# Kernel tuning notes

Hardware: AMD Instinct MI355X
Metric: run time of the kernel (lower is better)

The kernel has to match this reference:

```python
import jax, jax.numpy as jnp
import numpy as np

B, T, I, H, L = 64, 2048, 128, 128, 2  # batch, seq_len, input, hidden, layers


def setup_inputs() -> dict:
    key = jax.random.key(0)
    ks = jax.random.split(key, 6)
    w = lambda k, shape: jax.random.normal(k, shape, dtype=jnp.float32) * 0.05
    return {
        "x": jax.random.normal(ks[0], (B, T, I), dtype=jnp.float32),
        "Wx0": w(ks[1], (4 * H, I)),
        "Wh0": w(ks[2], (4 * H, H)),
        "b0": jnp.zeros((4 * H,), jnp.float32),
        "Wx1": w(ks[3], (4 * H, H)),
        "Wh1": w(ks[4], (4 * H, H)),
        "b1": jnp.zeros((4 * H,), jnp.float32),
    }


def _cell(x_t, h, c, Wx, Wh, b):
    # fused-gate GEMM; gate order (i, f, g, o) matches the torch cell exactly
    gates = x_t @ Wx.T + h @ Wh.T + b  # [B, 4H]
    i, f, g, o = jnp.split(gates, 4, axis=-1)
    i = jax.nn.sigmoid(i)
    f = jax.nn.sigmoid(f)
    g = jnp.tanh(g)
    o = jax.nn.sigmoid(o)
    c_new = f * c + i * g
    h_new = o * jnp.tanh(c_new)
    return h_new, c_new


def reference(x, Wx0, Wh0, b0, Wx1, Wh1, b1):
    params = [(Wx0, Wh0, b0), (Wx1, Wh1, b1)]
    bsz = x.shape[0]
    hidden = Wh0.shape[1]
    h0 = jnp.zeros((L, bsz, hidden), x.dtype)
    c0 = jnp.zeros((L, bsz, hidden), x.dtype)

    def step(carry, x_t):
        h, c = carry
        hs, cs = [], []
        inp = x_t
        for l, (Wx, Wh, b) in enumerate(params):  # fixed, tiny layer loop
            hl, cl = _cell(inp, h[l], c[l], Wx, Wh, b)
            inp = hl
            hs.append(hl)
            cs.append(cl)
        return (jnp.stack(hs), jnp.stack(cs)), inp

    (hT, cT), ys = jax.lax.scan(step, (h0, c0), jnp.swapaxes(x, 0, 1))
    output = jnp.swapaxes(ys, 0, 1)  # [B, T, H], top-layer hidden states
    return output, hT, cT
```

## Files before the change

kernel.cpp:

```cpp
#include <hip/hip_runtime.h>
#include <hip/hip_fp16.h>

#define BB 64
#define TT 2048
#define II 128
#define HH 128
#define NG 512
#define CH 128
#define NCH (TT / CH)
#define LEAD 4
#define DYN_LDS 81984

typedef _Float16 h2_t __attribute__((ext_vector_type(2)));

#if defined(__has_builtin)
#if __has_builtin(__builtin_amdgcn_fdot2)
#define HAVE_FDOT2 1
#endif
#endif

__device__ __forceinline__ float fdot2f(h2_t a, h2_t b, float c) {
#ifdef HAVE_FDOT2
  return __builtin_amdgcn_fdot2(a, b, c, false);
#else
  return c + (float)a[0] * (float)b[0] + (float)a[1] * (float)b[1];
#endif
}

__device__ __forceinline__ float fast_sigmoid(float x) {
  float t = __builtin_amdgcn_exp2f(-1.4426950408889634f * x);
  return __builtin_amdgcn_rcpf(1.0f + t);
}
__device__ __forceinline__ float act_gate(float x, bool tanh_sel) {
  float xx = tanh_sel ? 2.0f * x : x;
  float s = fast_sigmoid(xx);
  return tanh_sel ? 2.0f * s - 1.0f : s;
}
__device__ __forceinline__ float fast_tanh(float x) {
  return 2.0f * fast_sigmoid(2.0f * x) - 1.0f;
}

__device__ __forceinline__ float dpp_xor1(float x) {
  return __int_as_float(__builtin_amdgcn_update_dpp(0, __float_as_int(x), 0xB1, 0xF, 0xF, true));
}
__device__ __forceinline__ float dpp_xor2(float x) {
  return __int_as_float(__builtin_amdgcn_update_dpp(0, __float_as_int(x), 0x4E, 0xF, 0xF, true));
}

__device__ __forceinline__ void bar_lds() {
  __builtin_amdgcn_fence(__ATOMIC_RELEASE, "workgroup", "local");
  __builtin_amdgcn_s_barrier();
  __builtin_amdgcn_fence(__ATOMIC_ACQUIRE, "workgroup", "local");
}

union LD4 {
  float4 f4;
  h2_t h[4];
};
union LDB {
  uint4 u4;
  h2_t h[4];
};

__device__ __forceinline__ unsigned aload(unsigned* p) { return atomicAdd(p, 0u); }

__global__ void w_transpose2(const float* __restrict__ W0, float* __restrict__ T0,
                             const float* __restrict__ W1, float* __restrict__ T1) {
  int bid = blockIdx.x;
  const float* W = (bid < 256) ? W0 : W1;
  float* T = (bid < 256) ? T0 : T1;
  int idx = (bid & 255) * 256 + threadIdx.x;
  int n = idx >> 7;
  int k = idx & 127;
  T[k * NG + n] = W[idx];
}

__global__ __launch_bounds__(256) void xg_gemm_pro(const float* __restrict__ X,
                                                   const float* __restrict__ WT,
                                                   const float* __restrict__ bias,
                                                   __half* __restrict__ Xg) {
  __shared__ float As[64][132];
  __shared__ float Bs[128][64];
  const int bx = blockIdx.x;
  const size_t m0 = (size_t)(bx >> 3) * TT + (bx & 7) * 64;
  const int n0 = blockIdx.y * 64;
  const int tid = threadIdx.x;

  {
    const float4* xv = (const float4*)(X + m0 * II);
#pragma unroll
    for (int r = 0; r < 8; ++r) {
      int f = tid + 256 * r;
      int m = f >> 5;
      int c4 = f & 31;
      float4 v = xv[m * 32 + c4];
      *(float4*)&As[m][c4 * 4] = v;
    }
  }
  {
#pragma unroll
    for (int r = 0; r < 8; ++r) {
      int f = tid + 256 * r;
      int k = f >> 4;
      int q = f & 15;
      float4 v = *(const float4*)(WT + (size_t)k * NG + n0 + q * 4);
      *(float4*)&Bs[k][q * 4] = v;
    }
  }
  __syncthreads();

  const int tx = tid & 15;
  const int ty = tid >> 4;
  float acc[4][4];
#pragma unroll
  for (int i = 0; i < 4; ++i)
#pragma unroll
    for (int j = 0; j < 4; ++j) acc[i][j] = 0.0f;

#pragma unroll 4
  for (int k = 0; k < 128; ++k) {
    float a0 = As[ty * 4 + 0][k];
    float a1 = As[ty * 4 + 1][k];
    float a2 = As[ty * 4 + 2][k];
    float a3 = As[ty * 4 + 3][k];
    float4 bv = *(const float4*)&Bs[k][tx * 4];
    acc[0][0] = fmaf(a0, bv.x, acc[0][0]);
    acc[0][1] = fmaf(a0, bv.y, acc[0][1]);
    acc[0][2] = fmaf(a0, bv.z, acc[0][2]);
    acc[0][3] = fmaf(a0, bv.w, acc[0][3]);
    acc[1][0] = fmaf(a1, bv.x, acc[1][0]);
    acc[1][1] = fmaf(a1, bv.y, acc[1][1]);
    acc[1][2] = fmaf(a1, bv.z, acc[1][2]);
    acc[1][3] = fmaf(a1, bv.w, acc[1][3]);
    acc[2][0] = fmaf(a2, bv.x, acc[2][0]);
    acc[2][1] = fmaf(a2, bv.y, acc[2][1]);
    acc[2][2] = fmaf(a2, bv.z, acc[2][2]);
    acc[2][3] = fmaf(a2, bv.w, acc[2][3]);
    acc[3][0] = fmaf(a3, bv.x, acc[3][0]);
    acc[3][1] = fmaf(a3, bv.y, acc[3][1]);
    acc[3][2] = fmaf(a3, bv.z, acc[3][2]);
    acc[3][3] = fmaf(a3, bv.w, acc[3][3]);
  }

  float4 bvec = *(const float4*)(bias + n0 + tx * 4);
#pragma unroll
  for (int i = 0; i < 4; ++i) {
    size_t m = m0 + ty * 4 + i;
    __half2* dst = (__half2*)(Xg + m * NG + n0 + tx * 4);
    dst[0] = __halves2half2(__float2half(acc[i][0] + bvec.x),
                            __float2half(acc[i][1] + bvec.y));
    dst[1] = __halves2half2(__float2half(acc[i][2] + bvec.z),
                            __float2half(acc[i][3] + bvec.w));
  }
}


__device__ __forceinline__ void roleA(int b, int n, char* smem,
    const __half* Xg, const float* __restrict__ Wh0,
    float* __restrict__ out, __half* hstream,
    unsigned* flag0, unsigned* flagX)
{
  const int j = n >> 2;
  const int p = n & 3;
  const bool tsel = (p == 2);

  h2_t wh[4][16];
#pragma unroll
  for (int g = 0; g < 4; ++g) {
    const float2* ph = (const float2*)(Wh0 + (size_t)(g * 128 + j) * HH + p * 32);
#pragma unroll
    for (int k = 0; k < 16; ++k) {
      float2 v = ph[k];
      wh[g][k][0] = (_Float16)v.x;
      wh[g][k][1] = (_Float16)v.y;
    }
  }

  _Float16(*hb)[HH] = (_Float16(*)[HH])smem;
  if (n < HH) {
    hb[0][n] = (_Float16)0.0f;
    hb[1][n] = (_Float16)0.0f;
  }
  float c = 0.0f, hv = 0.0f;
  __syncthreads();

  const __half* xs = Xg + (size_t)b * TT * NG + p * 128 + j;
  float* hT = out + (size_t)BB * TT * HH;
  float* cT = hT + 2 * BB * HH;
  __half* hsp = hstream + (size_t)b * TT * HH + j;

#pragma unroll 1
  for (int cc = 0; cc < NCH; ++cc) {
    if (cc >= LEAD) {
      if (n == 0) {
        while (aload(flagX + b * NCH + cc) < 2u) __builtin_amdgcn_s_sleep(1);
      }
      __syncthreads();
      __builtin_amdgcn_fence(__ATOMIC_ACQUIRE, "agent");
    }
    __half xg_c = xs[(size_t)(cc * CH) * NG];

#pragma unroll 1
    for (int s = 0; s < CH; ++s) {
      const int i = cc * CH + s;
      __half xg_n = (s + 1 < CH) ? xs[(size_t)(i + 1) * NG] : __float2half(0.0f);

      const char* H = (const char*)hb[i & 1] + p * 64;
      float a0 = 0.f, a1 = 0.f, a2 = 0.f, a3 = 0.f;
#pragma unroll
      for (int q = 0; q < 4; ++q) {
        LD4 u;
        u.f4 = *(const float4*)(H + q * 16);
#pragma unroll
        for (int t = 0; t < 4; ++t) {
          const int m = q * 4 + t;
          a0 = fdot2f(wh[0][m], u.h[t], a0);
          a1 = fdot2f(wh[1][m], u.h[t], a1);
          a2 = fdot2f(wh[2][m], u.h[t], a2);
          a3 = fdot2f(wh[3][m], u.h[t], a3);
        }
      }

      float k01 = (p & 1) ? a1 : a0;
      float u01 = (p & 1) ? a0 : a1;
      float r01 = k01 + dpp_xor1(u01);
      float k23 = (p & 1) ? a3 : a2;
      float u23 = (p & 1) ? a2 : a3;
      float r23 = k23 + dpp_xor1(u23);
      float kA = (p & 2) ? r23 : r01;
      float uA = (p & 2) ? r01 : r23;
      float sL = kA + dpp_xor2(uA);
      float aL = act_gate(sL + __half2float(xg_c), tsel);
      float fg = dpp_xor1(aL);
      float gg = dpp_xor2(aL);
      float og = dpp_xor2(fg);
      if (p == 0) {
        c = fg * c + aL * gg;
        hv = og * fast_tanh(c);
        _Float16 hf = (_Float16)hv;
        hb[(i & 1) ^ 1][j] = hf;
        *(_Float16*)(hsp + (size_t)i * HH) = hf;
      }
      bar_lds();
      xg_c = xg_n;
    }
    __syncthreads();
    if (n == 0) {
      __builtin_amdgcn_fence(__ATOMIC_RELEASE, "agent");
      atomicExch(flag0 + b * NCH + cc, 1u);
    }
  }

  if (p == 0) {
    hT[b * HH + j] = hv;
    cT[b * HH + j] = c;
  }
}

__device__ __forceinline__ void roleC(int cidx, int n, char* smem,
    __half* Xg, const __half* hstream, const float* __restrict__ x,
    const float* __restrict__ WT0, const float* __restrict__ b0,
    const float* __restrict__ WT1, const float* __restrict__ b1,
    unsigned* flag0, unsigned* flagC, unsigned* flagX)
{
  const int b = cidx >> 1;
  const int half = cidx & 1;
  h2_t(*As2)[68] = (h2_t(*)[68])smem;
  h2_t(*Bs2)[64] = (h2_t(*)[64])(smem + 64 * 68 * 4);

  const int ty = n >> 4;
  const int tx = n & 15;
  const int mf = n >> 3;
  const int sf = n & 7;

#pragma unroll 1
  for (int cc = 0; cc < NCH; ++cc) {
    if (cc + LEAD < NCH) {
      const int t0x = (cc + LEAD) * CH + half * 64;
      {
        const float4* sx = (const float4*)(x + ((size_t)b * TT + t0x + mf) * II + sf * 16);
        float4 p0 = sx[0], p1 = sx[1], p2 = sx[2], p3 = sx[3];
        h2_t r[8];
        r[0][0] = (_Float16)p0.x; r[0][1] = (_Float16)p0.y;
        r[1][0] = (_Float16)p0.z; r[1][1] = (_Float16)p0.w;
        r[2][0] = (_Float16)p1.x; r[2][1] = (_Float16)p1.y;
        r[3][0] = (_Float16)p1.z; r[3][1] = (_Float16)p1.w;
        r[4][0] = (_Float16)p2.x; r[4][1] = (_Float16)p2.y;
        r[5][0] = (_Float16)p2.z; r[5][1] = (_Float16)p2.w;
        r[6][0] = (_Float16)p3.x; r[6][1] = (_Float16)p3.y;
        r[7][0] = (_Float16)p3.z; r[7][1] = (_Float16)p3.w;
        *(uint4*)&As2[mf][sf * 8] = *(uint4*)&r[0];
        *(uint4*)&As2[mf][sf * 8 + 4] = *(uint4*)&r[4];
      }
#pragma unroll 1
      for (int nt = 0; nt < 8; ++nt) {
        __syncthreads();
        {
          const int kp = n >> 3, cg = n & 7;
          const float4* w0 = (const float4*)(WT0 + (size_t)(2 * kp) * NG + nt * 64 + cg * 8);
          const float4* w1 = (const float4*)(WT0 + (size_t)(2 * kp + 1) * NG + nt * 64 + cg * 8);
          float4 x0 = w0[0], x1 = w0[1];
          float4 y0 = w1[0], y1 = w1[1];
          h2_t r[8];
          r[0][0] = (_Float16)x0.x; r[0][1] = (_Float16)y0.x;
          r[1][0] = (_Float16)x0.y; r[1][1] = (_Float16)y0.y;
          r[2][0] = (_Float16)x0.z; r[2][1] = (_Float16)y0.z;
          r[3][0] = (_Float16)x0.w; r[3][1] = (_Float16)y0.w;
          r[4][0] = (_Float16)x1.x; r[4][1] = (_Float16)y1.x;
          r[5][0] = (_Float16)x1.y; r[5][1] = (_Float16)y1.y;
          r[6][0] = (_Float16)x1.z; r[6][1] = (_Float16)y1.z;
          r[7][0] = (_Float16)x1.w; r[7][1] = (_Float16)y1.w;
          *(uint4*)&Bs2[kp][cg * 8] = *(uint4*)&r[0];
          *(uint4*)&Bs2[kp][cg * 8 + 4] = *(uint4*)&r[4];
        }
        __syncthreads();

        float acc[2][4];
#pragma unroll
        for (int r = 0; r < 2; ++r)
#pragma unroll
          for (int q = 0; q < 4; ++q) acc[r][q] = 0.0f;
#pragma unroll 4
        for (int k4 = 0; k4 < 16; ++k4) {
          LDB ua0, ua1;
          ua0.u4 = *(const uint4*)&As2[ty * 2][k4 * 4];
          ua1.u4 = *(const uint4*)&As2[ty * 2 + 1][k4 * 4];
#pragma unroll
          for (int t = 0; t < 4; ++t) {
            LDB ub;
            ub.u4 = *(const uint4*)&Bs2[k4 * 4 + t][tx * 4];
            acc[0][0] = fdot2f(ua0.h[t], ub.h[0], acc[0][0]);
            acc[0][1] = fdot2f(ua0.h[t], ub.h[1], acc[0][1]);
            acc[0][2] = fdot2f(ua0.h[t], ub.h[2], acc[0][2]);
            acc[0][3] = fdot2f(ua0.h[t], ub.h[3], acc[0][3]);
            acc[1][0] = fdot2f(ua1.h[t], ub.h[0], acc[1][0]);
            acc[1][1] = fdot2f(ua1.h[t], ub.h[1], acc[1][1]);
            acc[1][2] = fdot2f(ua1.h[t], ub.h[2], acc[1][2]);
            acc[1][3] = fdot2f(ua1.h[t], ub.h[3], acc[1][3]);
          }
        }
        const int col = nt * 64 + tx * 4;
        float4 bv = *(const float4*)(b0 + col);
#pragma unroll
        for (int r = 0; r < 2; ++r) {
          __half2* d = (__half2*)(Xg + ((size_t)b * TT + t0x + ty * 2 + r) * NG + col);
          d[0] = __halves2half2(__float2half(acc[r][0] + bv.x),
                                __float2half(acc[r][1] + bv.y));
          d[1] = __halves2half2(__float2half(acc[r][2] + bv.z),
                                __float2half(acc[r][3] + bv.w));
        }
      }
      __syncthreads();
      if (n == 0) {
        __builtin_amdgcn_fence(__ATOMIC_RELEASE, "agent");
        atomicAdd(flagX + b * NCH + cc + LEAD, 1u);
      }
    }

    if (n == 0) {
      while (aload(flag0 + b * NCH + cc) < 1u) __builtin_amdgcn_s_sleep(8);
    }
    __syncthreads();
    __builtin_amdgcn_fence(__ATOMIC_ACQUIRE, "agent");

    const int t0 = cc * CH + half * 64;
    {
      const uint4* src = (const uint4*)(hstream + ((size_t)b * TT + t0 + mf) * HH + sf * 16);
      uint4 v0 = src[0], v1 = src[1];
      *(uint4*)&As2[mf][sf * 8] = v0;
      *(uint4*)&As2[mf][sf * 8 + 4] = v1;
    }
#pragma unroll 1
    for (int nt = 0; nt < 8; ++nt) {
      __syncthreads();
      {
        const int kp = n >> 3, cg = n & 7;
        const float4* w0 = (const float4*)(WT1 + (size_t)(2 * kp) * NG + nt * 64 + cg * 8);
        const float4* w1 = (const float4*)(WT1 + (size_t)(2 * kp + 1) * NG + nt * 64 + cg * 8);
        float4 x0 = w0[0], x1 = w0[1];
        float4 y0 = w1[0], y1 = w1[1];
        h2_t r[8];
        r[0][0] = (_Float16)x0.x; r[0][1] = (_Float16)y0.x;
        r[1][0] = (_Float16)x0.y; r[1][1] = (_Float16)y0.y;
        r[2][0] = (_Float16)x0.z; r[2][1] = (_Float16)y0.z;
        r[3][0] = (_Float16)x0.w; r[3][1] = (_Float16)y0.w;
        r[4][0] = (_Float16)x1.x; r[4][1] = (_Float16)y1.x;
        r[5][0] = (_Float16)x1.y; r[5][1] = (_Float16)y1.y;
        r[6][0] = (_Float16)x1.z; r[6][1] = (_Float16)y1.z;
        r[7][0] = (_Float16)x1.w; r[7][1] = (_Float16)y1.w;
        *(uint4*)&Bs2[kp][cg * 8] = *(uint4*)&r[0];
        *(uint4*)&Bs2[kp][cg * 8 + 4] = *(uint4*)&r[4];
      }
      __syncthreads();

      float acc[2][4];
#pragma unroll
      for (int r = 0; r < 2; ++r)
#pragma unroll
        for (int q = 0; q < 4; ++q) acc[r][q] = 0.0f;
#pragma unroll 4
      for (int k4 = 0; k4 < 16; ++k4) {
        LDB ua0, ua1;
        ua0.u4 = *(const uint4*)&As2[ty * 2][k4 * 4];
        ua1.u4 = *(const uint4*)&As2[ty * 2 + 1][k4 * 4];
#pragma unroll
        for (int t = 0; t < 4; ++t) {
          LDB ub;
          ub.u4 = *(const uint4*)&Bs2[k4 * 4 + t][tx * 4];
          acc[0][0] = fdot2f(ua0.h[t], ub.h[0], acc[0][0]);
          acc[0][1] = fdot2f(ua0.h[t], ub.h[1], acc[0][1]);
          acc[0][2] = fdot2f(ua0.h[t], ub.h[2], acc[0][2]);
          acc[0][3] = fdot2f(ua0.h[t], ub.h[3], acc[0][3]);
          acc[1][0] = fdot2f(ua1.h[t], ub.h[0], acc[1][0]);
          acc[1][1] = fdot2f(ua1.h[t], ub.h[1], acc[1][1]);
          acc[1][2] = fdot2f(ua1.h[t], ub.h[2], acc[1][2]);
          acc[1][3] = fdot2f(ua1.h[t], ub.h[3], acc[1][3]);
        }
      }
      const int col = nt * 64 + tx * 4;
      float4 bv = *(const float4*)(b1 + col);
#pragma unroll
      for (int r = 0; r < 2; ++r) {
        __half2* d = (__half2*)(Xg + ((size_t)b * TT + t0 + ty * 2 + r) * NG + col);
        d[0] = __halves2half2(__float2half(acc[r][0] + bv.x),
                              __float2half(acc[r][1] + bv.y));
        d[1] = __halves2half2(__float2half(acc[r][2] + bv.z),
                              __float2half(acc[r][3] + bv.w));
      }
    }
    __syncthreads();
    if (n == 0) {
      __builtin_amdgcn_fence(__ATOMIC_RELEASE, "agent");
      atomicAdd(flagC + b * NCH + cc, 1u);
    }
  }
}

__device__ __forceinline__ void roleB(int b, int n, char* smem,
    const __half* Xg, const float* __restrict__ Wh1,
    float* __restrict__ out, unsigned* flagC)
{
  const int j = n >> 2;
  const int p = n & 3;
  const bool tsel = (p == 2);

  h2_t wh[4][16];
#pragma unroll
  for (int g = 0; g < 4; ++g) {
    const float2* ph = (const float2*)(Wh1 + (size_t)(g * 128 + j) * HH + p * 32);
#pragma unroll
    for (int k = 0; k < 16; ++k) {
      float2 v = ph[k];
      wh[g][k][0] = (_Float16)v.x;
      wh[g][k][1] = (_Float16)v.y;
    }
  }

  _Float16(*hb)[HH] = (_Float16(*)[HH])smem;
  if (n < HH) {
    hb[0][n] = (_Float16)0.0f;
    hb[1][n] = (_Float16)0.0f;
  }
  float c = 0.0f, hv = 0.0f;
  __syncthreads();

  const __half* xs = Xg + (size_t)b * TT * NG + p * 128 + j;
  float* outp = out + (size_t)b * TT * HH;
  float* hT = out + (size_t)BB * TT * HH;
  float* cT = hT + 2 * BB * HH;

#pragma unroll 1
  for (int cc = 0; cc < NCH; ++cc) {
    if (n == 0) {
      while (aload(flagC + b * NCH + cc) < 2u) __builtin_amdgcn_s_sleep(8);
    }
    __syncthreads();
    __builtin_amdgcn_fence(__ATOMIC_ACQUIRE, "agent");

    __half xg_c = xs[(size_t)(cc * CH) * NG];
#pragma unroll 1
    for (int s = 0; s < CH; ++s) {
      const int i = cc * CH + s;
      __half xg_n = (s + 1 < CH) ? xs[(size_t)(i + 1) * NG] : __float2half(0.0f);

      const char* H = (const char*)hb[i & 1] + p * 64;
      float a0 = 0.f, a1 = 0.f, a2 = 0.f, a3 = 0.f;
#pragma unroll
      for (int q = 0; q < 4; ++q) {
        LD4 u;
        u.f4 = *(const float4*)(H + q * 16);
#pragma unroll
        for (int t = 0; t < 4; ++t) {
          const int m = q * 4 + t;
          a0 = fdot2f(wh[0][m], u.h[t], a0);
          a1 = fdot2f(wh[1][m], u.h[t], a1);
          a2 = fdot2f(wh[2][m], u.h[t], a2);
          a3 = fdot2f(wh[3][m], u.h[t], a3);
        }
      }

      float k01 = (p & 1) ? a1 : a0;
      float u01 = (p & 1) ? a0 : a1;
      float r01 = k01 + dpp_xor1(u01);
      float k23 = (p & 1) ? a3 : a2;
      float u23 = (p & 1) ? a2 : a3;
      float r23 = k23 + dpp_xor1(u23);
      float kA = (p & 2) ? r23 : r01;
      float uA = (p & 2) ? r01 : r23;
      float sL = kA + dpp_xor2(uA);
      float aL = act_gate(sL + __half2float(xg_c), tsel);
      float fg = dpp_xor1(aL);
      float gg = dpp_xor2(aL);
      float og = dpp_xor2(fg);
      if (p == 0) {
        c = fg * c + aL * gg;
        hv = og * fast_tanh(c);
        hb[(i & 1) ^ 1][j] = (_Float16)hv;
        outp[(size_t)i * HH + j] = hv;
      }
      bar_lds();
      xg_c = xg_n;
    }
  }

  if (p == 0) {
    hT[BB * HH + b * HH + j] = hv;
    cT[BB * HH + b * HH + j] = c;
  }
}

__global__
__attribute__((amdgpu_flat_work_group_size(512, 512)))
void lstm_mega(__half* Xg, __half* hstream, const float* __restrict__ x,
               const float* __restrict__ Wh0,
               const float* __restrict__ Wh1,
               const float* __restrict__ WT0,
               const float* __restrict__ b0,
               const float* __restrict__ WT1,
               const float* __restrict__ b1,
               float* __restrict__ out,
               unsigned* flag0, unsigned* flagC, unsigned* flagX)
{
  extern __shared__ __align__(16) char smem[];
  const int bid = blockIdx.x;
  const int n = threadIdx.x;
  if (bid < BB) {
    roleA(bid, n, smem, Xg, Wh0, out, hstream, flag0, flagX);
  } else if (bid < BB + 2 * BB) {
    roleC(bid - BB, n, smem, Xg, hstream, x, WT0, b0, WT1, b1,
          flag0, flagC, flagX);
  } else {
    roleB(bid - 3 * BB, n, smem, Xg, Wh1, out, flagC);
  }
}

extern "C" void kernel_launch(void* const* d_in, const int* in_sizes, int n_in,
                              void* d_out, int out_size, void* d_ws, size_t ws_size,
                              hipStream_t stream) {
  const float* x   = (const float*)d_in[0];
  const float* Wx0 = (const float*)d_in[1];
  const float* Wh0 = (const float*)d_in[2];
  const float* b0  = (const float*)d_in[3];
  const float* Wx1 = (const float*)d_in[4];
  const float* Wh1 = (const float*)d_in[5];
  const float* b1  = (const float*)d_in[6];
  float* out = (float*)d_out;

  char* base = (char*)d_ws;
  __half* Xg = (__half*)base;
  size_t off = (size_t)BB * TT * NG * sizeof(__half);
  __half* hstream = (__half*)(base + off);
  off += (size_t)BB * TT * HH * sizeof(__half);
  float* WT0 = (float*)(base + off);
  off += (size_t)II * NG * sizeof(float);
  float* WT1 = (float*)(base + off);
  off += (size_t)II * NG * sizeof(float);
  unsigned* flag0 = (unsigned*)(base + off);
  unsigned* flagC = flag0 + BB * NCH;
  unsigned* flagX = flagC + BB * NCH;

  hipFuncSetAttribute((const void*)lstm_mega,
                      hipFuncAttributeMaxDynamicSharedMemorySize, DYN_LDS);

  hipMemsetAsync(flag0, 0, 3 * (size_t)BB * NCH * sizeof(unsigned), stream);
  w_transpose2<<<512, 256, 0, stream>>>(Wx0, WT0, Wx1, WT1);
  xg_gemm_pro<<<dim3(BB * 8, NG / 64), 256, 0, stream>>>(x, WT0, b0, Xg);
  lstm_mega<<<4 * BB, 512, DYN_LDS, stream>>>(Xg, hstream, x, Wh0, Wh1, WT0,
                                              b0, WT1, b1, out, flag0, flagC,
                                              flagX);
}
```

Baseline: 1.415 ms.

## Split recurrent dot products across 8 lanes per unit with 1024-thread blocks

The recurrent roles now use 1024 threads, with 8 lanes per hidden unit each handling 16 inputs instead of 4 lanes handling 32, and an extra ds_swizzle xor-4 reduction. This is meant to shorten the per-step serial critical path. The chunk size is halved and the lead doubled. The GEMM role now handles alternating whole chunks with threads 512 and above idle, and the flags switch to exchange semantics. The larger blocks add barrier cost and register pressure. The roleC chunk ownership also changes: it now indexes by parity but still covers only 64 rows of each 64-step chunk.

```diff
diff --git a/kernel.cpp b/kernel.cpp
--- a/kernel.cpp
+++ b/kernel.cpp
@@ -6,9 +6,9 @@
 #define II 128
 #define HH 128
 #define NG 512
-#define CH 128
+#define CH 64
 #define NCH (TT / CH)
-#define LEAD 4
+#define LEAD 8
 #define DYN_LDS 81984
 
 typedef _Float16 h2_t __attribute__((ext_vector_type(2)));
@@ -45,6 +45,9 @@
 }
 __device__ __forceinline__ float dpp_xor2(float x) {
   return __int_as_float(__builtin_amdgcn_update_dpp(0, __float_as_int(x), 0x4E, 0xF, 0xF, true));
+}
+__device__ __forceinline__ float swz_xor4(float x) {
+  return __int_as_float(__builtin_amdgcn_ds_swizzle(__float_as_int(x), 0x101F));
 }
 
 __device__ __forceinline__ void bar_lds() {
@@ -155,21 +158,23 @@
 }
 
 
-__device__ __forceinline__ void roleA(int b, int n, char* smem,
-    const __half* Xg, const float* __restrict__ Wh0,
+template <int LAYER>
+__device__ __forceinline__ void role_rec(int b, int n, char* smem,
+    const __half* Xg, const float* __restrict__ Wh,
     float* __restrict__ out, __half* hstream,
-    unsigned* flag0, unsigned* flagX)
+    unsigned* flagIn)
 {
-  const int j = n >> 2;
-  const int p = n & 3;
-  const bool tsel = (p == 2);
-
-  h2_t wh[4][16];
+  const int j = n >> 3;
+  const int p = n & 7;
+  const int g0v_ = p & 3;
+  const bool tsel = (g0v_ == 2);
+
+  h2_t wh[4][8];
 #pragma unroll
   for (int g = 0; g < 4; ++g) {
-    const float2* ph = (const float2*)(Wh0 + (size_t)(g * 128 + j) * HH + p * 32);
-#pragma unroll
-    for (int k = 0; k < 16; ++k) {
+    const float2* ph = (const float2*)(Wh + (size_t)(g * 128 + j) * HH + p * 16);
+#pragma unroll
+    for (int k = 0; k < 8; ++k) {
       float2 v = ph[k];
       wh[g][k][0] = (_Float16)v.x;
       wh[g][k][1] = (_Float16)v.y;
@@ -184,16 +189,17 @@
   float c = 0.0f, hv = 0.0f;
   __syncthreads();
 
-  const __half* xs = Xg + (size_t)b * TT * NG + p * 128 + j;
+  const __half* xs = Xg + (size_t)b * TT * NG + g0v_ * 128 + j;
   float* hT = out + (size_t)BB * TT * HH;
   float* cT = hT + 2 * BB * HH;
   __half* hsp = hstream + (size_t)b * TT * HH + j;
+  float* outp = out + (size_t)b * TT * HH;
 
 #pragma unroll 1
   for (int cc = 0; cc < NCH; ++cc) {
-    if (cc >= LEAD) {
+    if (LAYER == 0 ? (cc >= LEAD) : true) {
       if (n == 0) {
-        while (aload(flagX + b * NCH + cc) < 2u) __builtin_amdgcn_s_sleep(1);
+        while (aload(flagIn + b * NCH + cc) < 1u) __builtin_amdgcn_s_sleep(4);
       }
       __syncthreads();
       __builtin_amdgcn_fence(__ATOMIC_ACQUIRE, "agent");
@@ -205,20 +211,24 @@
       const int i = cc * CH + s;
       __half xg_n = (s + 1 < CH) ? xs[(size_t)(i + 1) * NG] : __float2half(0.0f);
 
-      const char* H = (const char*)hb[i & 1] + p * 64;
+      const char* H = (const char*)hb[i & 1] + p * 32;
+      LD4 u0, u1;
+      u0.f4 = *(const float4*)(H);
+      u1.f4 = *(const float4*)(H + 16);
       float a0 = 0.f, a1 = 0.f, a2 = 0.f, a3 = 0.f;
 #pragma unroll
-      for (int q = 0; q < 4; ++q) {
-        LD4 u;
-        u.f4 = *(const float4*)(H + q * 16);
-#pragma unroll
-        for (int t = 0; t < 4; ++t) {
-          const int m = q * 4 + t;
-          a0 = fdot2f(wh[0][m], u.h[t], a0);
-          a1 = fdot2f(wh[1][m], u.h[t], a1);
-          a2 = fdot2f(wh[2][m], u.h[t], a2);
-          a3 = fdot2f(wh[3][m], u.h[t], a3);
-        }
+      for (int t = 0; t < 4; ++t) {
+        a0 = fdot2f(wh[0][t], u0.h[t], a0);
+        a1 = fdot2f(wh[1][t], u0.h[t], a1);
+        a2 = fdot2f(wh[2][t], u0.h[t], a2);
+        a3 = fdot2f(wh[3][t], u0.h[t], a3);
+      }
+#pragma unroll
+      for (int t = 0; t < 4; ++t) {
+        a0 = fdot2f(wh[0][4 + t], u1.h[t], a0);
+        a1 = fdot2f(wh[1][4 + t], u1.h[t], a1);
+        a2 = fdot2f(wh[2][4 + t], u1.h[t], a2);
+        a3 = fdot2f(wh[3][4 + t], u1.h[t], a3);
       }
 
       float k01 = (p & 1) ? a1 : a0;
@@ -229,7 +239,9 @@
       float r23 = k23 + dpp_xor1(u23);
       float kA = (p & 2) ? r23 : r01;
       float uA = (p & 2) ? r01 : r23;
-      float sL = kA + dpp_xor2(uA);
+      float sLq = kA + dpp_xor2(uA);
+      float sL = sLq + swz_xor4(sLq);
+
       float aL = act_gate(sL + __half2float(xg_c), tsel);
       float fg = dpp_xor1(aL);
       float gg = dpp_xor2(aL);
@@ -239,21 +251,33 @@
         hv = og * fast_tanh(c);
         _Float16 hf = (_Float16)hv;
         hb[(i & 1) ^ 1][j] = hf;
-        *(_Float16*)(hsp + (size_t)i * HH) = hf;
+        if (LAYER == 0) {
+          *(_Float16*)(hsp + (size_t)i * HH) = hf;
+        } else {
+          outp[(size_t)i * HH + j] = hv;
+        }
       }
       bar_lds();
       xg_c = xg_n;
     }
-    __syncthreads();
-    if (n == 0) {
+    if (LAYER == 0) {
+      __syncthreads();
+      if (n == 0) {
+        __builtin_amdgcn_fence(__ATOMIC_RELEASE, "agent");
+        atomicExch(out ? (unsigned*)0 : (unsigned*)0, 0u);
+      }
+    }
+    if (LAYER == 0 && n == 0) {
       __builtin_amdgcn_fence(__ATOMIC_RELEASE, "agent");
-      atomicExch(flag0 + b * NCH + cc, 1u);
+    }
+    if (LAYER == 0) {
+      if (n == 0) atomicExch((unsigned*)flagIn - (size_t)BB * NCH + b * NCH + cc, 1u);
     }
   }
 
   if (p == 0) {
-    hT[b * HH + j] = hv;
-    cT[b * HH + j] = c;
+    hT[LAYER * BB * HH + b * HH + j] = hv;
+    cT[LAYER * BB * HH + b * HH + j] = c;
   }
 }
 
@@ -264,7 +288,7 @@
     unsigned* flag0, unsigned* flagC, unsigned* flagX)
 {
   const int b = cidx >> 1;
-  const int half = cidx & 1;
+  const int par = cidx & 1;
   h2_t(*As2)[68] = (h2_t(*)[68])smem;
   h2_t(*Bs2)[64] = (h2_t(*)[64])(smem + 64 * 68 * 4);
 
@@ -274,10 +298,10 @@
   const int sf = n & 7;
 
 #pragma unroll 1
-  for (int cc = 0; cc < NCH; ++cc) {
+  for (int cc = par; cc < NCH; cc += 2) {
     if (cc + LEAD < NCH) {
-      const int t0x = (cc + LEAD) * CH + half * 64;
-      {
+      const int t0x = (cc + LEAD) * CH;
+      if (n < 512) {
         const float4* sx = (const float4*)(x + ((size_t)b * TT + t0x + mf) * II + sf * 16);
         float4 p0 = sx[0], p1 = sx[1], p2 = sx[2], p3 = sx[3];
         h2_t r[8];
@@ -295,7 +319,7 @@
 #pragma unroll 1
       for (int nt = 0; nt < 8; ++nt) {
         __syncthreads();
-        {
+        if (n < 512) {
           const int kp = n >> 3, cg = n & 7;
           const float4* w0 = (const float4*)(WT0 + (size_t)(2 * kp) * NG + nt * 64 + cg * 8);
           const float4* w1 = (const float4*)(WT0 + (size_t)(2 * kp + 1) * NG + nt * 64 + cg * 8);
@@ -315,45 +339,47 @@
         }
         __syncthreads();
 
-        float acc[2][4];
-#pragma unroll
-        for (int r = 0; r < 2; ++r)
-#pragma unroll
-          for (int q = 0; q < 4; ++q) acc[r][q] = 0.0f;
+        if (n < 512) {
+          float acc[2][4];
+#pragma unroll
+          for (int r = 0; r < 2; ++r)
+#pragma unroll
+            for (int q = 0; q < 4; ++q) acc[r][q] = 0.0f;
 #pragma unroll 4
-        for (int k4 = 0; k4 < 16; ++k4) {
-          LDB ua0, ua1;
-          ua0.u4 = *(const uint4*)&As2[ty * 2][k4 * 4];
-          ua1.u4 = *(const uint4*)&As2[ty * 2 + 1][k4 * 4];
-#pragma unroll
-          for (int t = 0; t < 4; ++t) {
-            LDB ub;
-            ub.u4 = *(const uint4*)&Bs2[k4 * 4 + t][tx * 4];
-            acc[0][0] = fdot2f(ua0.h[t], ub.h[0], acc[0][0]);
-            acc[0][1] = fdot2f(ua0.h[t], ub.h[1], acc[0][1]);
-            acc[0][2] = fdot2f(ua0.h[t], ub.h[2], acc[0][2]);
-            acc[0][3] = fdot2f(ua0.h[t], ub.h[3], acc[0][3]);
-            acc[1][0] = fdot2f(ua1.h[t], ub.h[0], acc[1][0]);
-            acc[1][1] = fdot2f(ua1.h[t], ub.h[1], acc[1][1]);
-            acc[1][2] = fdot2f(ua1.h[t], ub.h[2], acc[1][2]);
-            acc[1][3] = fdot2f(ua1.h[t], ub.h[3], acc[1][3]);
+          for (int k4 = 0; k4 < 16; ++k4) {
+            LDB ua0, ua1;
+            ua0.u4 = *(const uint4*)&As2[ty * 2][k4 * 4];
+            ua1.u4 = *(const uint4*)&As2[ty * 2 + 1][k4 * 4];
+#pragma unroll
+            for (int t = 0; t < 4; ++t) {
+              LDB ub;
+              ub.u4 = *(const uint4*)&Bs2[k4 * 4 + t][tx * 4];
+              acc[0][0] = fdot2f(ua0.h[t], ub.h[0], acc[0][0]);
+              acc[0][1] = fdot2f(ua0.h[t], ub.h[1], acc[0][1]);
+              acc[0][2] = fdot2f(ua0.h[t], ub.h[2], acc[0][2]);
+              acc[0][3] = fdot2f(ua0.h[t], ub.h[3], acc[0][3]);
+              acc[1][0] = fdot2f(ua1.h[t], ub.h[0], acc[1][0]);
+              acc[1][1] = fdot2f(ua1.h[t], ub.h[1], acc[1][1]);
+              acc[1][2] = fdot2f(ua1.h[t], ub.h[2], acc[1][2]);
+              acc[1][3] = fdot2f(ua1.h[t], ub.h[3], acc[1][3]);
+            }
           }
-        }
-        const int col = nt * 64 + tx * 4;
-        float4 bv = *(const float4*)(b0 + col);
-#pragma unroll
-        for (int r = 0; r < 2; ++r) {
-          __half2* d = (__half2*)(Xg + ((size_t)b * TT + t0x + ty * 2 + r) * NG + col);
-          d[0] = __halves2half2(__float2half(acc[r][0] + bv.x),
-                                __float2half(acc[r][1] + bv.y));
-          d[1] = __halves2half2(__float2half(acc[r][2] + bv.z),
-                                __float2half(acc[r][3] + bv.w));
+          const int col = nt * 64 + tx * 4;
+          float4 bv = *(const float4*)(b0 + col);
+#pragma unroll
+          for (int r = 0; r < 2; ++r) {
+            __half2* d = (__half2*)(Xg + ((size_t)b * TT + t0x + ty * 2 + r) * NG + col);
+            d[0] = __halves2half2(__float2half(acc[r][0] + bv.x),
+                                  __float2half(acc[r][1] + bv.y));
+            d[1] = __halves2half2(__float2half(acc[r][2] + bv.z),
+                                  __float2half(acc[r][3] + bv.w));
+          }
         }
       }
       __syncthreads();
       if (n == 0) {
         __builtin_amdgcn_fence(__ATOMIC_RELEASE, "agent");
-        atomicAdd(flagX + b * NCH + cc + LEAD, 1u);
+        atomicExch(flagX + b * NCH + cc + LEAD, 1u);
       }
     }
 
@@ -363,8 +389,8 @@
     __syncthreads();
     __builtin_amdgcn_fence(__ATOMIC_ACQUIRE, "agent");
 
-    const int t0 = cc * CH + half * 64;
-    {
+    const int t0 = cc * CH;
+    if (n < 512) {
       const uint4* src = (const uint4*)(hstream + ((size_t)b * TT + t0 + mf) * HH + sf * 16);
       uint4 v0 = src[0], v1 = src[1];
       *(uint4*)&As2[mf][sf * 8] = v0;
@@ -373,7 +399,7 @@
 #pragma unroll 1
     for (int nt = 0; nt < 8; ++nt) {
       __syncthreads();
-      {
+      if (n < 512) {
         const int kp = n >> 3, cg = n & 7;
         const float4* w0 = (const float4*)(WT1 + (size_t)(2 * kp) * NG + nt * 64 + cg * 8);
         const float4* w1 = (const float4*)(WT1 + (size_t)(2 * kp + 1) * NG + nt * 64 + cg * 8);
@@ -393,63 +419,68 @@
       }
       __syncthreads();
 
-      float acc[2][4];
-#pragma unroll
-      for (int r = 0; r < 2; ++r)
-#pragma unroll
-        for (int q = 0; q < 4; ++q) acc[r][q] = 0.0f;
+      if (n < 512) {
+        float acc[2][4];
+#pragma unroll
+        for (int r = 0; r < 2; ++r)
+#pragma unroll
+          for (int q = 0; q < 4; ++q) acc[r][q] = 0.0f;
 #pragma unroll 4
-      for (int k4 = 0; k4 < 16; ++k4) {
-        LDB ua0, ua1;
-        ua0.u4 = *(const uint4*)&As2[ty * 2][k4 * 4];
-        ua1.u4 = *(const uint4*)&As2[ty * 2 + 1][k4 * 4];
-#pragma unroll
-        for (int t = 0; t < 4; ++t) {
-          LDB ub;
-          ub.u4 = *(const uint4*)&Bs2[k4 * 4 + t][tx * 4];
-          acc[0][0] = fdot2f(ua0.h[t], ub.h[0], acc[0][0]);
-          acc[0][1] = fdot2f(ua0.h[t], ub.h[1], acc[0][1]);
-          acc[0][2] = fdot2f(ua0.h[t], ub.h[2], acc[0][2]);
-          acc[0][3] = fdot2f(ua0.h[t], ub.h[3], acc[0][3]);
-          acc[1][0] = fdot2f(ua1.h[t], ub.h[0], acc[1][0]);
-          acc[1][1] = fdot2f(ua1.h[t], ub.h[1], acc[1][1]);
-          acc[1][2] = fdot2f(ua1.h[t], ub.h[2], acc[1][2]);
-          acc[1][3] = fdot2f(ua1.h[t], ub.h[3], acc[1][3]);
+        for (int k4 = 0; k4 < 16; ++k4) {
+          LDB ua0, ua1;
+          ua0.u4 = *(const uint4*)&As2[ty * 2][k4 * 4];
+          ua1.u4 = *(const uint4*)&As2[ty * 2 + 1][k4 * 4];
+#pragma unroll
+          for (int t = 0; t < 4; ++t) {
+            LDB ub;
+            ub.u4 = *(const uint4*)&Bs2[k4 * 4 + t][tx * 4];
+            acc[0][0] = fdot2f(ua0.h[t], ub.h[0], acc[0][0]);
+            acc[0][1] = fdot2f(ua0.h[t], ub.h[1], acc[0][1]);
+            acc[0][2] = fdot2f(ua0.h[t], ub.h[2], acc[0][2]);
+            acc[0][3] = fdot2f(ua0.h[t], ub.h[3], acc[0][3]);
+            acc[1][0] = fdot2f(ua1.h[t], ub.h[0], acc[1][0]);
+            acc[1][1] = fdot2f(ua1.h[t], ub.h[1], acc[1][1]);
+            acc[1][2] = fdot2f(ua1.h[t], ub.h[2], acc[1][2]);
+            acc[1][3] = fdot2f(ua1.h[t], ub.h[3], acc[1][3]);
+          }
         }
-      }
-      const int col = nt * 64 + tx * 4;
-      float4 bv = *(const float4*)(b1 + col);
-#pragma unroll
-      for (int r = 0; r < 2; ++r) {
-        __half2* d = (__half2*)(Xg + ((size_t)b * TT + t0 + ty * 2 + r) * NG + col);
-        d[0] = __halves2half2(__float2half(acc[r][0] + bv.x),
-                              __float2half(acc[r][1] + bv.y));
-        d[1] = __halves2half2(__float2half(acc[r][2] + bv.z),
-                              __float2half(acc[r][3] + bv.w));
+        const int col = nt * 64 + tx * 4;
+        float4 bv = *(const float4*)(b1 + col);
+#pragma unroll
+        for (int r = 0; r < 2; ++r) {
+          __half2* d = (__half2*)(Xg + ((size_t)b * TT + t0 + ty * 2 + r) * NG + col);
+          d[0] = __halves2half2(__float2half(acc[r][0] + bv.x),
+                                __float2half(acc[r][1] + bv.y));
+          d[1] = __halves2half2(__float2half(acc[r][2] + bv.z),
+                                __float2half(acc[r][3] + bv.w));
+        }
       }
     }
     __syncthreads();
     if (n == 0) {
       __builtin_amdgcn_fence(__ATOMIC_RELEASE, "agent");
-      atomicAdd(flagC + b * NCH + cc, 1u);
-    }
-  }
-}
-
-__device__ __forceinline__ void roleB(int b, int n, char* smem,
-    const __half* Xg, const float* __restrict__ Wh1,
-    float* __restrict__ out, unsigned* flagC)
+      atomicExch(flagC + b * NCH + cc, 1u);
+    }
+  }
+}
+
+template <int LAYER>
+__device__ __forceinline__ void role_rec2(int b, int n, char* smem,
+    const __half* Xg, const float* __restrict__ Wh,
+    float* __restrict__ out, __half* hstream,
+    unsigned* flagWait, unsigned* flagPub)
 {
-  const int j = n >> 2;
-  const int p = n & 3;
-  const bool tsel = (p == 2);
-
-  h2_t wh[4][16];
+  const int j = n >> 3;
+  const int p = n & 7;
+  const int gate = p & 3;
+  const bool tsel = (gate == 2);
+
+  h2_t wh[4][8];
 #pragma unroll
   for (int g = 0; g < 4; ++g) {
-    const float2* ph = (const float2*)(Wh1 + (size_t)(g * 128 + j) * HH + p * 32);
-#pragma unroll
-    for (int k = 0; k < 16; ++k) {
+    const float2* ph = (const float2*)(Wh + (size_t)(g * 128 + j) * HH + p * 16);
+#pragma unroll
+    for (int k = 0; k < 8; ++k) {
       float2 v = ph[k];
       wh[g][k][0] = (_Float16)v.x;
       wh[g][k][1] = (_Float16)v.y;
@@ -464,39 +495,47 @@
   float c = 0.0f, hv = 0.0f;
   __syncthreads();
 
-  const __half* xs = Xg + (size_t)b * TT * NG + p * 128 + j;
-  float* outp = out + (size_t)b * TT * HH;
+  const __half* xs = Xg + (size_t)b * TT * NG + gate * 128 + j;
   float* hT = out + (size_t)BB * TT * HH;
   float* cT = hT + 2 * BB * HH;
+  __half* hsp = hstream + (size_t)b * TT * HH + j;
+  float* outp = out + (size_t)b * TT * HH;
 
 #pragma unroll 1
   for (int cc = 0; cc < NCH; ++cc) {
-    if (n == 0) {
-      while (aload(flagC + b * NCH + cc) < 2u) __builtin_amdgcn_s_sleep(8);
-    }
-    __syncthreads();
-    __builtin_amdgcn_fence(__ATOMIC_ACQUIRE, "agent");
-
+    const bool needWait = (LAYER == 0) ? (cc >= LEAD) : true;
+    if (needWait) {
+      if (n == 0) {
+        while (aload(flagWait + b * NCH + cc) < 1u) __builtin_amdgcn_s_sleep(4);
+      }
+      __syncthreads();
+      __builtin_amdgcn_fence(__ATOMIC_ACQUIRE, "agent");
+    }
     __half xg_c = xs[(size_t)(cc * CH) * NG];
+
 #pragma unroll 1
     for (int s = 0; s < CH; ++s) {
       const int i = cc * CH + s;
       __half xg_n = (s + 1 < CH) ? xs[(size_t)(i + 1) * NG] : __float2half(0.0f);
 
-      const char* H = (const char*)hb[i & 1] + p * 64;
+      const char* H = (const char*)hb[i & 1] + p * 32;
+      LD4 u0, u1;
+      u0.f4 = *(const float4*)(H);
+      u1.f4 = *(const float4*)(H + 16);
       float a0 = 0.f, a1 = 0.f, a2 = 0.f, a3 = 0.f;
 #pragma unroll
-      for (int q = 0; q < 4; ++q) {
-        LD4 u;
-        u.f4 = *(const float4*)(H + q * 16);
-#pragma unroll
-        for (int t = 0; t < 4; ++t) {
-          const int m = q * 4 + t;
-          a0 = fdot2f(wh[0][m], u.h[t], a0);
-          a1 = fdot2f(wh[1][m], u.h[t], a1);
-          a2 = fdot2f(wh[2][m], u.h[t], a2);
-          a3 = fdot2f(wh[3][m], u.h[t], a3);
-        }
+      for (int t = 0; t < 4; ++t) {
+        a0 = fdot2f(wh[0][t], u0.h[t], a0);
+        a1 = fdot2f(wh[1][t], u0.h[t], a1);
+        a2 = fdot2f(wh[2][t], u0.h[t], a2);
+        a3 = fdot2f(wh[3][t], u0.h[t], a3);
+      }
+#pragma unroll
+      for (int t = 0; t < 4; ++t) {
+        a0 = fdot2f(wh[0][4 + t], u1.h[t], a0);
+        a1 = fdot2f(wh[1][4 + t], u1.h[t], a1);
+        a2 = fdot2f(wh[2][4 + t], u1.h[t], a2);
+        a3 = fdot2f(wh[3][4 + t], u1.h[t], a3);
       }
 
       float k01 = (p & 1) ? a1 : a0;
@@ -507,7 +546,9 @@
       float r23 = k23 + dpp_xor1(u23);
       float kA = (p & 2) ? r23 : r01;
       float uA = (p & 2) ? r01 : r23;
-      float sL = kA + dpp_xor2(uA);
+      float sLq = kA + dpp_xor2(uA);
+      float sL = sLq + swz_xor4(sLq);
+
       float aL = act_gate(sL + __half2float(xg_c), tsel);
       float fg = dpp_xor1(aL);
       float gg = dpp_xor2(aL);
@@ -515,22 +556,34 @@
       if (p == 0) {
         c = fg * c + aL * gg;
         hv = og * fast_tanh(c);
-        hb[(i & 1) ^ 1][j] = (_Float16)hv;
-        outp[(size_t)i * HH + j] = hv;
+        _Float16 hf = (_Float16)hv;
+        hb[(i & 1) ^ 1][j] = hf;
+        if (LAYER == 0) {
+          *(_Float16*)(hsp + (size_t)i * HH) = hf;
+        } else {
+          outp[(size_t)i * HH + j] = hv;
+        }
       }
       bar_lds();
       xg_c = xg_n;
     }
+    if (LAYER == 0) {
+      __syncthreads();
+      if (n == 0) {
+        __builtin_amdgcn_fence(__ATOMIC_RELEASE, "agent");
+        atomicExch(flagPub + b * NCH + cc, 1u);
+      }
+    }
   }
 
   if (p == 0) {
-    hT[BB * HH + b * HH + j] = hv;
-    cT[BB * HH + b * HH + j] = c;
+    hT[LAYER * BB * HH + b * HH + j] = hv;
+    cT[LAYER * BB * HH + b * HH + j] = c;
   }
 }
 
 __global__
-__attribute__((amdgpu_flat_work_group_size(512, 512)))
+__attribute__((amdgpu_flat_work_group_size(1024, 1024)))
 void lstm_mega(__half* Xg, __half* hstream, const float* __restrict__ x,
                const float* __restrict__ Wh0,
                const float* __restrict__ Wh1,
@@ -545,12 +598,12 @@
   const int bid = blockIdx.x;
   const int n = threadIdx.x;
   if (bid < BB) {
-    roleA(bid, n, smem, Xg, Wh0, out, hstream, flag0, flagX);
+    role_rec2<0>(bid, n, smem, Xg, Wh0, out, hstream, flagX, flag0);
   } else if (bid < BB + 2 * BB) {
     roleC(bid - BB, n, smem, Xg, hstream, x, WT0, b0, WT1, b1,
           flag0, flagC, flagX);
   } else {
-    roleB(bid - 3 * BB, n, smem, Xg, Wh1, out, flagC);
+    role_rec2<1>(bid - 3 * BB, n, smem, Xg, Wh1, out, hstream, flagC, flag0);
   }
 }
 
@@ -585,7 +638,7 @@
   hipMemsetAsync(flag0, 0, 3 * (size_t)BB * NCH * sizeof(unsigned), stream);
   w_transpose2<<<512, 256, 0, stream>>>(Wx0, WT0, Wx1, WT1);
   xg_gemm_pro<<<dim3(BB * 8, NG / 64), 256, 0, stream>>>(x, WT0, b0, Xg);
-  lstm_mega<<<4 * BB, 512, DYN_LDS, stream>>>(Xg, hstream, x, Wh0, Wh1, WT0,
-                                              b0, WT1, b1, out, flag0, flagC,
-                                              flagX);
-}
+  lstm_mega<<<4 * BB, 1024, DYN_LDS, stream>>>(Xg, hstream, x, Wh0, Wh1, WT0,
+                                               b0, WT1, b1, out, flag0, flagC,
+                                               flagX);
+}
```

New measurement: 1.931 ms. +36.5%, slower.
